# Kernel optimization log

Hardware: AMD Instinct MI355X
Metric: run time of the kernel (lower is better)

Reference implementation:

```python
import jax, jax.numpy as jnp
import numpy as np

N_NODES = 50000
N_EDGES = 800000
NODE_DIM = 128
EDGE_DIM = 16
OUT_DIM = 64
HEADS = 4


def setup_inputs() -> dict:
    key = jax.random.key(0)
    ks = jax.random.split(key, 12)
    x = jax.random.normal(ks[0], (N_NODES, NODE_DIM), jnp.float32)
    edge_index = jax.random.randint(ks[1], (2, N_EDGES), 0, N_NODES)
    batch = jnp.zeros((N_NODES,), jnp.int32)
    edge_attr = jax.random.normal(ks[2], (N_EDGES, EDGE_DIM), jnp.float32)
    s = 1.0 / np.sqrt(NODE_DIM)
    W = jax.random.normal(ks[3], (NODE_DIM, HEADS * OUT_DIM), jnp.float32) * s
    att_src = jax.random.normal(ks[4], (HEADS, OUT_DIM), jnp.float32) * 0.1
    att_dst = jax.random.normal(ks[5], (HEADS, OUT_DIM), jnp.float32) * 0.1
    W_e = jax.random.normal(ks[6], (EDGE_DIM, HEADS * OUT_DIM), jnp.float32) * (1.0 / np.sqrt(EDGE_DIM))
    att_edge = jax.random.normal(ks[7], (HEADS, OUT_DIM), jnp.float32) * 0.1
    bias = jnp.zeros((OUT_DIM,), jnp.float32)
    gamma = jnp.ones((OUT_DIM,), jnp.float32)
    beta = jnp.zeros((OUT_DIM,), jnp.float32)
    return {"x": x, "edge_index": edge_index, "batch": batch, "edge_attr": edge_attr,
            "W": W, "att_src": att_src, "att_dst": att_dst, "W_e": W_e,
            "att_edge": att_edge, "bias": bias, "gamma": gamma, "beta": beta}


def reference(x, edge_index, batch, edge_attr, W, att_src, att_dst, W_e, att_edge, bias, gamma, beta):
    N = x.shape[0]
    H, C = att_src.shape
    src, dst = edge_index[0], edge_index[1]
    E = src.shape[0]

    # add self loops; self-loop edge_attr = per-node mean of incoming edge attrs (PyG fill_value='mean')
    cnt = jax.ops.segment_sum(jnp.ones((E, 1), x.dtype), dst, num_segments=N)
    loop_attr = jax.ops.segment_sum(edge_attr, dst, num_segments=N) / jnp.maximum(cnt, 1.0)
    loop_idx = jnp.arange(N, dtype=src.dtype)
    src_f = jnp.concatenate([src, loop_idx])
    dst_f = jnp.concatenate([dst, loop_idx])
    ea = jnp.concatenate([edge_attr, loop_attr], axis=0)

    h = (x @ W).reshape(N, H, C)                       # [N,H,C]
    a_src = jnp.einsum('nhc,hc->nh', h, att_src)       # [N,H]
    a_dst = jnp.einsum('nhc,hc->nh', h, att_dst)
    e_emb = (ea @ W_e).reshape(-1, H, C)               # [E',H,C]
    a_edge = jnp.einsum('ehc,hc->eh', e_emb, att_edge)

    alpha = jax.nn.leaky_relu(a_src[src_f] + a_dst[dst_f] + a_edge, 0.2)  # [E',H]
    amax = jax.ops.segment_max(alpha, dst_f, num_segments=N)
    expa = jnp.exp(alpha - amax[dst_f])
    denom = jax.ops.segment_sum(expa, dst_f, num_segments=N)
    att = expa / (denom[dst_f] + 1e-16)                # segment softmax over dst

    msg = h[src_f] * att[:, :, None]                   # [E',H,C]
    out = jax.ops.segment_sum(msg, dst_f, num_segments=N)  # [N,H,C]
    out = out.mean(axis=1) + bias                      # concat=False -> head mean

    mu = out.mean(-1, keepdims=True)
    var = out.var(-1, keepdims=True)
    out = (out - mu) / jnp.sqrt(var + 1e-5) * gamma + beta
    return jax.nn.elu(out)
```

## Files before the change

kernel.cpp:

```cpp
#include <hip/hip_runtime.h>

typedef unsigned int u32;
typedef unsigned short u16;

static constexpr int NN  = 50000;
static constexpr int EE  = 800000;
static constexpr int CAP = 64;

typedef __attribute__((ext_vector_type(8))) short bf16x8;
typedef __attribute__((ext_vector_type(4))) float f32x4;

__device__ inline float u2f(u32 u){ union{u32 i; float f;} v; v.i=u; return v.f; }
__device__ inline float bf2f(u16 u){ return u2f(((u32)u)<<16); }
__device__ inline u16 f2bf(float f){ union{float f; u32 i;} v; v.f=f; u32 i=v.i;
    return (u16)((i + 0x7fffu + ((i>>16)&1u))>>16); }
__device__ inline u32 pk2(float a, float b){ return (u32)f2bf(a) | ((u32)f2bf(b)<<16); }
__device__ inline float lrelu(float x){ return x > 0.f ? x : 0.2f*x; }

__device__ inline float ld(const void* base, size_t i, int f32m){
    return f32m ? ((const float*)base)[i] : bf2f(((const u16*)base)[i]);
}

__device__ inline float wsum(float v){
    #pragma unroll
    for (int m=1;m<64;m<<=1) v += __shfl_xor(v, m, 64);
    return v;
}

#if defined(__has_builtin)
#if __has_builtin(__builtin_amdgcn_fdot2_f32_bf16)
#define HAS_DOT2 1
#endif
#endif

#ifdef HAS_DOT2
typedef __attribute__((ext_vector_type(2))) __bf16 bf16x2;
#endif

__device__ inline float dot2acc(u32 hv, u32 wv, float acc){
#ifdef HAS_DOT2
    union { u32 u; bf16x2 v; } a, b; a.u = hv; b.u = wv;
    return __builtin_amdgcn_fdot2_f32_bf16(a.v, b.v, acc, false);
#else
    acc = fmaf(u2f(hv<<16),         u2f(wv<<16),         acc);
    acc = fmaf(u2f(hv&0xffff0000u), u2f(wv&0xffff0000u), acc);
    return acc;
#endif
}

__device__ inline int detect_f32(const u16* xraw){
    int lane = threadIdx.x & 63;
    bool bad = false;
    #pragma unroll
    for (int i = 0; i < 8; ++i){
        float v = bf2f(xraw[2*(lane + i*64)]);
        if (!(fabsf(v) < 1e10f)) bad = true;
    }
    return __any(bad) ? 1 : 0;
}

__device__ inline void edge_logits(const void* ea, int e, int f32m,
                                   const float* Ml, float* A){
    float v[16];
    if (f32m){
        const float4* r = ((const float4*)ea) + (size_t)e*4;
        float4 a = r[0], b = r[1], c = r[2], d = r[3];
        v[0]=a.x; v[1]=a.y; v[2]=a.z; v[3]=a.w;
        v[4]=b.x; v[5]=b.y; v[6]=b.z; v[7]=b.w;
        v[8]=c.x; v[9]=c.y; v[10]=c.z; v[11]=c.w;
        v[12]=d.x; v[13]=d.y; v[14]=d.z; v[15]=d.w;
    } else {
        const uint4* r = ((const uint4*)ea) + (size_t)e*2;
        uint4 q0 = r[0], q1 = r[1];
        v[0]=u2f(q0.x<<16); v[1]=u2f(q0.x&0xffff0000u);
        v[2]=u2f(q0.y<<16); v[3]=u2f(q0.y&0xffff0000u);
        v[4]=u2f(q0.z<<16); v[5]=u2f(q0.z&0xffff0000u);
        v[6]=u2f(q0.w<<16); v[7]=u2f(q0.w&0xffff0000u);
        v[8]=u2f(q1.x<<16); v[9]=u2f(q1.x&0xffff0000u);
        v[10]=u2f(q1.y<<16); v[11]=u2f(q1.y&0xffff0000u);
        v[12]=u2f(q1.z<<16); v[13]=u2f(q1.z&0xffff0000u);
        v[14]=u2f(q1.w<<16); v[15]=u2f(q1.w&0xffff0000u);
    }
    float a0=0,a1=0,a2=0,a3=0;
    #pragma unroll
    for (int j = 0; j < 16; ++j){
        a0 = fmaf(v[j], Ml[j*4+0], a0);
        a1 = fmaf(v[j], Ml[j*4+1], a1);
        a2 = fmaf(v[j], Ml[j*4+2], a2);
        a3 = fmaf(v[j], Ml[j*4+3], a3);
    }
    A[0]=a0; A[1]=a1; A[2]=a2; A[3]=a3;
}

__global__ __launch_bounds__(256) void k_prep(const u16* __restrict__ xraw,
                                              const void* __restrict__ W,
                                              const void* __restrict__ att_src,
                                              const void* __restrict__ att_dst,
                                              const void* __restrict__ W_e,
                                              const void* __restrict__ att_edge,
                                              int* __restrict__ flag,
                                              u16* __restrict__ Wt,
                                              float* __restrict__ Mv){
    int f32m = detect_f32(xraw);
    int b = blockIdx.x, t = threadIdx.x;
    if (b == 0){
        if (t == 0) *flag = f32m;
        if (t < 64){
            int d = t >> 2, h = t & 3;
            float s = 0.f;
            for (int c = 0; c < 64; ++c)
                s += ld(W_e, d*256 + h*64 + c, f32m) * ld(att_edge, h*64 + c, f32m);
            Mv[t] = s;
        }
    } else if (b <= 128){
        int i = (b-1)*256 + t;
        int k = i >> 8, n = i & 255;
        Wt[n*128 + k] = f2bf(ld(W, (size_t)k*256 + n, f32m));
    } else {
        int i = (b-129)*256 + t;
        int c = i >> 7, k = i & 127;
        float s = 0.f;
        if (c < 8){
            int h = c & 3;
            const void* att = (c < 4) ? att_src : att_dst;
            for (int j = 0; j < 64; ++j)
                s += ld(W, (size_t)k*256 + h*64 + j, f32m) * ld(att, h*64 + j, f32m);
        }
        Wt[(size_t)(256 + c)*128 + k] = f2bf(s);
    }
}

static constexpr int LDSROW = 136;
static constexpr int CROW   = 264;

__global__ __launch_bounds__(256) void k_gemm(const void* __restrict__ x,
                                              const u16* __restrict__ Wt,
                                              const int* __restrict__ flag,
                                              u16* __restrict__ hbuf,
                                              float* __restrict__ a_src,
                                              float* __restrict__ a_dst, int N){
    __shared__ u16 sh[64*CROW];
    int f32m = *flag;
    int t = threadIdx.x;
    int row0 = blockIdx.x*64;
    if (f32m){
        const float4* xg = (const float4*)x;
        #pragma unroll
        for (int j=0;j<8;++j){
            int idx = t + j*256;
            int r = idx >> 5, c4 = idx & 31;
            int gr = row0 + r; if (gr >= N) gr = N-1;
            float4 v = xg[(size_t)gr*32 + c4];
            *(uint2*)&sh[r*LDSROW + c4*4] = make_uint2(pk2(v.x,v.y), pk2(v.z,v.w));
        }
    } else {
        const uint4* xg = (const uint4*)x;
        #pragma unroll
        for (int j=0;j<4;++j){
            int idx = t + j*256;
            int r = idx >> 4, c8 = idx & 15;
            int gr = row0 + r; if (gr >= N) gr = N-1;
            uint4 v = xg[(size_t)gr*16 + c8];
            *(uint4*)&sh[r*LDSROW + c8*8] = v;
        }
    }
    __syncthreads();
    int wave = t >> 6, lane = t & 63;
    int l15 = lane & 15, quad = lane >> 4;
    int mrow = wave*16 + l15;
    bf16x8 afr[4];
    #pragma unroll
    for (int s=0;s<4;++s)
        afr[s] = *(const bf16x8*)&sh[mrow*LDSROW + s*32 + quad*8];
    __syncthreads();
    f32x4 acc[17];
    #pragma unroll
    for (int tl=0;tl<17;++tl){
        f32x4 a = {0.f,0.f,0.f,0.f};
        #pragma unroll
        for (int s=0;s<4;++s){
            bf16x8 bfr = *(const bf16x8*)&Wt[(size_t)(tl*16 + l15)*128 + s*32 + quad*8];
            a = __builtin_amdgcn_mfma_f32_16x16x32_bf16(afr[s], bfr, a, 0, 0, 0);
        }
        acc[tl] = a;
    }
    int rbase = row0 + wave*16 + quad*4;
    #pragma unroll
    for (int r=0;r<4;++r){
        int gr = rbase + r;
        if (gr < N){
            if (l15 < 4)      a_src[gr*4 + l15]     = acc[16][r];
            else if (l15 < 8) a_dst[gr*4 + (l15-4)] = acc[16][r];
        }
    }
    #pragma unroll
    for (int r=0;r<4;++r){
        int row = wave*16 + quad*4 + r;
        #pragma unroll
        for (int tl=0;tl<4;++tl){
            u32 lo = pk2(acc[tl  ][r], acc[tl+4 ][r]);
            u32 hi = pk2(acc[tl+8][r], acc[tl+12][r]);
            *(uint2*)&sh[row*CROW + (tl*16 + l15)*4] = make_uint2(lo, hi);
        }
    }
    __syncthreads();
    uint4* h4 = (uint4*)hbuf;
    #pragma unroll
    for (int j=0;j<8;++j){
        int idx = t + j*256;
        int row = idx >> 5, c16 = idx & 31;
        if (row0 + row < N){
            uint4 v = *(const uint4*)&sh[row*CROW + c16*8];
            h4[(size_t)(row0 + row)*32 + c16] = v;
        }
    }
}

__global__ __launch_bounds__(256) void k_edge(const int* __restrict__ ei,
                                              const void* __restrict__ ea,
                                              const float* __restrict__ Mv,
                                              const int* __restrict__ flag,
                                              const float* __restrict__ a_src,
                                              const float* __restrict__ a_dst,
                                              int* __restrict__ deg,
                                              uint4* __restrict__ brec,
                                              u32* __restrict__ ba23, int E){
    __shared__ float Ml[64];
    if (threadIdx.x < 64) Ml[threadIdx.x] = Mv[threadIdx.x];
    __syncthreads();
    int f32m = *flag;
    int base = blockIdx.x*1024 + threadIdx.x;
    int e[4], src[4], dst[4];
    bool val[4];
    float A[4][4];
    #pragma unroll
    for (int j=0;j<4;++j){
        e[j] = base + j*256;
        val[j] = e[j] < E;
        int ec = val[j] ? e[j] : 0;
        src[j] = ei[ec];
        dst[j] = ei[E + ec];
        edge_logits(ea, ec, f32m, Ml, A[j]);
    }
    float4 as[4], ad[4];
    #pragma unroll
    for (int j=0;j<4;++j){
        as[j] = ((const float4*)a_src)[src[j]];
        ad[j] = ((const float4*)a_dst)[dst[j]];
    }
    #pragma unroll
    for (int j=0;j<4;++j){
        if (!val[j]) continue;
        float w0 = expf(lrelu(as[j].x + ad[j].x + A[j][0]));
        float w1 = expf(lrelu(as[j].y + ad[j].y + A[j][1]));
        float w2 = expf(lrelu(as[j].z + ad[j].z + A[j][2]));
        float w3 = expf(lrelu(as[j].w + ad[j].w + A[j][3]));
        int slot = atomicAdd(&deg[dst[j]], 1);
        if (slot < CAP){
            int idx = dst[j]*CAP + slot;
            brec[idx] = make_uint4((u32)src[j], pk2(w0,w1), pk2(w2,w3), pk2(A[j][0],A[j][1]));
            ba23[idx] = pk2(A[j][2],A[j][3]);
        }
    }
}

__global__ __launch_bounds__(256) void k_node(const int* __restrict__ deg,
                                              const uint4* __restrict__ brec,
                                              const u32* __restrict__ ba23,
                                              const float* __restrict__ a_src,
                                              const float* __restrict__ a_dst,
                                              const u16* __restrict__ hbuf,
                                              const void* __restrict__ bias,
                                              const void* __restrict__ gamma,
                                              const void* __restrict__ beta,
                                              const int* __restrict__ flag,
                                              void* __restrict__ out, int N){
    __shared__ uint4 lrec[4][CAP+4];
    int f32m = *flag;
    int lane = threadIdx.x & 63;
    int slot = threadIdx.x >> 6;
    int n = blockIdx.x*4 + slot;
    int dg = deg[n];
    int dc = dg < CAP ? dg : CAP;
    float4 an = ((const float4*)a_src)[n];
    float4 ad = ((const float4*)a_dst)[n];
    bool v0 = lane < dc;
    u32 src = (u32)n;
    float w0=0.f,w1=0.f,w2=0.f,w3=0.f;
    float a0=0.f,a1=0.f,a2=0.f,a3=0.f;
    if (v0){
        uint4 r = brec[(size_t)n*CAP + lane];
        u32 q = ba23[(size_t)n*CAP + lane];
        src = r.x;
        w0 = u2f(r.y<<16); w1 = u2f(r.y&0xffff0000u);
        w2 = u2f(r.z<<16); w3 = u2f(r.z&0xffff0000u);
        a0 = u2f(r.w<<16); a1 = u2f(r.w&0xffff0000u);
        a2 = u2f(q<<16);   a3 = u2f(q&0xffff0000u);
    }
    float dn0 = wsum(w0), dn1 = wsum(w1), dn2 = wsum(w2), dn3 = wsum(w3);
    float invd = 1.f / (float)(dg > 1 ? dg : 1);
    float ge0 = wsum(a0)*invd, ge1 = wsum(a1)*invd;
    float ge2 = wsum(a2)*invd, ge3 = wsum(a3)*invd;
    float exS0 = expf(lrelu(an.x + ad.x + ge0));
    float exS1 = expf(lrelu(an.y + ad.y + ge1));
    float exS2 = expf(lrelu(an.z + ad.z + ge2));
    float exS3 = expf(lrelu(an.w + ad.w + ge3));
    float i0 = 0.25f/(dn0 + exS0 + 1e-16f);
    float i1 = 0.25f/(dn1 + exS1 + 1e-16f);
    float i2 = 0.25f/(dn2 + exS2 + 1e-16f);
    float i3 = 0.25f/(dn3 + exS3 + 1e-16f);
    if (v0)
        lrec[slot][lane] = make_uint4(src, pk2(w0*i0, w1*i1), pk2(w2*i2, w3*i3), 0u);
    if (lane == 0)
        lrec[slot][dc] = make_uint4((u32)n, pk2(exS0*i0, exS1*i1), pk2(exS2*i2, exS3*i3), 0u);
    else if (lane <= 3)
        lrec[slot][dc + lane] = make_uint4((u32)n, 0u, 0u, 0u);
    __syncthreads();
    int T = dc + 1;
    int iters = (T + 3) >> 2;
    int half = lane >> 5, l5 = lane & 31;
    const uint4* hb4 = (const uint4*)hbuf;
    float acc0 = 0.f, acc1 = 0.f;
    uint4 r0 = lrec[slot][half];
    uint4 r1 = lrec[slot][2 + half];
    uint4 h0 = hb4[(size_t)r0.x*32 + l5];
    uint4 h1 = hb4[(size_t)r1.x*32 + l5];
    for (int i = 1; i < iters; ++i){
        uint4 nr0 = lrec[slot][4*i + half];
        uint4 nr1 = lrec[slot][4*i + 2 + half];
        uint4 nh0 = hb4[(size_t)nr0.x*32 + l5];
        uint4 nh1 = hb4[(size_t)nr1.x*32 + l5];
        acc0 = dot2acc(h0.x, r0.y, acc0);
        acc0 = dot2acc(h0.y, r0.z, acc0);
        acc1 = dot2acc(h0.z, r0.y, acc1);
        acc1 = dot2acc(h0.w, r0.z, acc1);
        acc0 = dot2acc(h1.x, r1.y, acc0);
        acc0 = dot2acc(h1.y, r1.z, acc0);
        acc1 = dot2acc(h1.z, r1.y, acc1);
        acc1 = dot2acc(h1.w, r1.z, acc1);
        r0 = nr0; r1 = nr1; h0 = nh0; h1 = nh1;
    }
    acc0 = dot2acc(h0.x, r0.y, acc0);
    acc0 = dot2acc(h0.y, r0.z, acc0);
    acc1 = dot2acc(h0.z, r0.y, acc1);
    acc1 = dot2acc(h0.w, r0.z, acc1);
    acc0 = dot2acc(h1.x, r1.y, acc0);
    acc0 = dot2acc(h1.y, r1.z, acc0);
    acc1 = dot2acc(h1.z, r1.y, acc1);
    acc1 = dot2acc(h1.w, r1.z, acc1);
    acc0 += __shfl_xor(acc0, 32, 64);
    acc1 += __shfl_xor(acc1, 32, 64);
    float va = __shfl(acc0, lane>>1, 64);
    float vb = __shfl(acc1, lane>>1, 64);
    float o = ((lane & 1) ? vb : va) + ld(bias, lane, f32m);
    float mu = wsum(o) * (1.f/64.f);
    float d = o - mu;
    float var = wsum(d*d) * (1.f/64.f);
    float y = d * rsqrtf(var + 1e-5f) * ld(gamma, lane, f32m) + ld(beta, lane, f32m);
    y = y > 0.f ? y : expf(y) - 1.f;
    if (f32m) ((float*)out)[(size_t)n*64 + lane] = y;
    else      ((u16*)out)[(size_t)n*64 + lane] = f2bf(y);
}

extern "C" void kernel_launch(void* const* d_in, const int* in_sizes, int n_in,
                              void* d_out, int out_size, void* d_ws, size_t ws_size,
                              hipStream_t stream){
    const void* x        = d_in[0];
    const int*  ei       = (const int*)d_in[1];
    const void* ea       = d_in[3];
    const void* W        = d_in[4];
    const void* att_src  = d_in[5];
    const void* att_dst  = d_in[6];
    const void* W_e      = d_in[7];
    const void* att_edge = d_in[8];
    const void* bias     = d_in[9];
    const void* gamma    = d_in[10];
    const void* beta     = d_in[11];
    const int N = NN, E = EE;

    char* p = (char*)d_ws;
    auto alloc = [&](size_t bytes){ void* r = (void*)p; p += (bytes + 255) & ~(size_t)255; return r; };
    int*   deg   = (int*)  alloc((size_t)N*4);
    float* Mv    = (float*)alloc(64*4);
    float* a_src = (float*)alloc((size_t)N*16);
    float* a_dst = (float*)alloc((size_t)N*16);
    uint4* brec  = (uint4*)alloc((size_t)N*CAP*16);
    u32*   ba23  = (u32*)  alloc((size_t)N*CAP*4);
    u16*   hbuf  = (u16*)  alloc((size_t)N*256*2);
    u16*   Wt    = (u16*)  alloc((size_t)272*128*2);
    int*   flag  = (int*)  alloc(256);

    hipMemsetAsync(deg, 0, (size_t)N*4, stream);
    k_prep<<<137, 256, 0, stream>>>((const u16*)x, W, att_src, att_dst, W_e, att_edge,
                                    flag, Wt, Mv);
    k_gemm<<<(N+63)/64, 256, 0, stream>>>(x, Wt, flag, hbuf, a_src, a_dst, N);
    k_edge<<<(E+1023)/1024, 256, 0, stream>>>(ei, ea, Mv, flag, a_src, a_dst,
                                              deg, brec, ba23, E);
    k_node<<<N/4, 256, 0, stream>>>(deg, brec, ba23, a_src, a_dst, hbuf,
                                    bias, gamma, beta, flag, d_out, N);
}
```

Measured before the change: 302.6 us.

## Move edge exp weights into node kernel and shrink bucket records to 12 bytes

The edge kernel no longer gathers a_src/a_dst or computes exp weights. It stores only src plus four fp16 edge logits per bucketed record, packed into 12 bytes instead of 16+4. The node kernel now gathers a_src[src] per edge and computes the exponentials there. Streaming inputs use nontemporal loads, and the edge kernel handles 2 edges per thread instead of 4. This cuts bucket write/read traffic and the random gathers in k_edge, at the cost of a random gather in k_node, unaligned 3-word records, and fp16 precision for the logits.

```diff
diff --git a/kernel.cpp b/kernel.cpp
--- a/kernel.cpp
+++ b/kernel.cpp
@@ -9,6 +9,7 @@
 
 typedef __attribute__((ext_vector_type(8))) short bf16x8;
 typedef __attribute__((ext_vector_type(4))) float f32x4;
+typedef __attribute__((ext_vector_type(4))) u32   u32x4;
 
 __device__ inline float u2f(u32 u){ union{u32 i; float f;} v; v.i=u; return v.f; }
 __device__ inline float bf2f(u16 u){ return u2f(((u32)u)<<16); }
@@ -16,6 +17,14 @@
     return (u16)((i + 0x7fffu + ((i>>16)&1u))>>16); }
 __device__ inline u32 pk2(float a, float b){ return (u32)f2bf(a) | ((u32)f2bf(b)<<16); }
 __device__ inline float lrelu(float x){ return x > 0.f ? x : 0.2f*x; }
+
+__device__ inline u32 pkh(float a, float b){
+    union{ _Float16 h[2]; u32 u; } v;
+    v.h[0] = (_Float16)a; v.h[1] = (_Float16)b;
+    return v.u;
+}
+__device__ inline float hlo(u32 u){ union{u32 u; _Float16 h[2];} v; v.u=u; return (float)v.h[0]; }
+__device__ inline float hhi(u32 u){ union{u32 u; _Float16 h[2];} v; v.u=u; return (float)v.h[1]; }
 
 __device__ inline float ld(const void* base, size_t i, int f32m){
     return f32m ? ((const float*)base)[i] : bf2f(((const u16*)base)[i]);
@@ -63,23 +72,27 @@
                                    const float* Ml, float* A){
     float v[16];
     if (f32m){
-        const float4* r = ((const float4*)ea) + (size_t)e*4;
-        float4 a = r[0], b = r[1], c = r[2], d = r[3];
-        v[0]=a.x; v[1]=a.y; v[2]=a.z; v[3]=a.w;
-        v[4]=b.x; v[5]=b.y; v[6]=b.z; v[7]=b.w;
-        v[8]=c.x; v[9]=c.y; v[10]=c.z; v[11]=c.w;
-        v[12]=d.x; v[13]=d.y; v[14]=d.z; v[15]=d.w;
+        const f32x4* r = ((const f32x4*)ea) + (size_t)e*4;
+        f32x4 a = __builtin_nontemporal_load(r);
+        f32x4 b = __builtin_nontemporal_load(r+1);
+        f32x4 c = __builtin_nontemporal_load(r+2);
+        f32x4 d = __builtin_nontemporal_load(r+3);
+        v[0]=a[0]; v[1]=a[1]; v[2]=a[2]; v[3]=a[3];
+        v[4]=b[0]; v[5]=b[1]; v[6]=b[2]; v[7]=b[3];
+        v[8]=c[0]; v[9]=c[1]; v[10]=c[2]; v[11]=c[3];
+        v[12]=d[0]; v[13]=d[1]; v[14]=d[2]; v[15]=d[3];
     } else {
-        const uint4* r = ((const uint4*)ea) + (size_t)e*2;
-        uint4 q0 = r[0], q1 = r[1];
-        v[0]=u2f(q0.x<<16); v[1]=u2f(q0.x&0xffff0000u);
-        v[2]=u2f(q0.y<<16); v[3]=u2f(q0.y&0xffff0000u);
-        v[4]=u2f(q0.z<<16); v[5]=u2f(q0.z&0xffff0000u);
-        v[6]=u2f(q0.w<<16); v[7]=u2f(q0.w&0xffff0000u);
-        v[8]=u2f(q1.x<<16); v[9]=u2f(q1.x&0xffff0000u);
-        v[10]=u2f(q1.y<<16); v[11]=u2f(q1.y&0xffff0000u);
-        v[12]=u2f(q1.z<<16); v[13]=u2f(q1.z&0xffff0000u);
-        v[14]=u2f(q1.w<<16); v[15]=u2f(q1.w&0xffff0000u);
+        const u32x4* r = ((const u32x4*)ea) + (size_t)e*2;
+        u32x4 q0 = __builtin_nontemporal_load(r);
+        u32x4 q1 = __builtin_nontemporal_load(r+1);
+        v[0]=u2f(q0[0]<<16); v[1]=u2f(q0[0]&0xffff0000u);
+        v[2]=u2f(q0[1]<<16); v[3]=u2f(q0[1]&0xffff0000u);
+        v[4]=u2f(q0[2]<<16); v[5]=u2f(q0[2]&0xffff0000u);
+        v[6]=u2f(q0[3]<<16); v[7]=u2f(q0[3]&0xffff0000u);
+        v[8]=u2f(q1[0]<<16); v[9]=u2f(q1[0]&0xffff0000u);
+        v[10]=u2f(q1[1]<<16); v[11]=u2f(q1[1]&0xffff0000u);
+        v[12]=u2f(q1[2]<<16); v[13]=u2f(q1[2]&0xffff0000u);
+        v[14]=u2f(q1[3]<<16); v[15]=u2f(q1[3]&0xffff0000u);
     }
     float a0=0,a1=0,a2=0,a3=0;
     #pragma unroll
@@ -144,24 +157,24 @@
     int t = threadIdx.x;
     int row0 = blockIdx.x*64;
     if (f32m){
-        const float4* xg = (const float4*)x;
+        const f32x4* xg = (const f32x4*)x;
         #pragma unroll
         for (int j=0;j<8;++j){
             int idx = t + j*256;
             int r = idx >> 5, c4 = idx & 31;
             int gr = row0 + r; if (gr >= N) gr = N-1;
-            float4 v = xg[(size_t)gr*32 + c4];
-            *(uint2*)&sh[r*LDSROW + c4*4] = make_uint2(pk2(v.x,v.y), pk2(v.z,v.w));
+            f32x4 v = __builtin_nontemporal_load(&xg[(size_t)gr*32 + c4]);
+            *(uint2*)&sh[r*LDSROW + c4*4] = make_uint2(pk2(v[0],v[1]), pk2(v[2],v[3]));
         }
     } else {
-        const uint4* xg = (const uint4*)x;
+        const u32x4* xg = (const u32x4*)x;
         #pragma unroll
         for (int j=0;j<4;++j){
             int idx = t + j*256;
             int r = idx >> 4, c8 = idx & 15;
             int gr = row0 + r; if (gr >= N) gr = N-1;
-            uint4 v = xg[(size_t)gr*16 + c8];
-            *(uint4*)&sh[r*LDSROW + c8*8] = v;
+            u32x4 v = __builtin_nontemporal_load(&xg[(size_t)gr*16 + c8]);
+            *(u32x4*)&sh[r*LDSROW + c8*8] = v;
         }
     }
     __syncthreads();
@@ -220,53 +233,33 @@
                                               const void* __restrict__ ea,
                                               const float* __restrict__ Mv,
                                               const int* __restrict__ flag,
-                                              const float* __restrict__ a_src,
-                                              const float* __restrict__ a_dst,
                                               int* __restrict__ deg,
-                                              uint4* __restrict__ brec,
-                                              u32* __restrict__ ba23, int E){
+                                              u32* __restrict__ brec, int E){
     __shared__ float Ml[64];
     if (threadIdx.x < 64) Ml[threadIdx.x] = Mv[threadIdx.x];
     __syncthreads();
     int f32m = *flag;
-    int base = blockIdx.x*1024 + threadIdx.x;
-    int e[4], src[4], dst[4];
-    bool val[4];
-    float A[4][4];
-    #pragma unroll
-    for (int j=0;j<4;++j){
-        e[j] = base + j*256;
-        val[j] = e[j] < E;
-        int ec = val[j] ? e[j] : 0;
-        src[j] = ei[ec];
-        dst[j] = ei[E + ec];
-        edge_logits(ea, ec, f32m, Ml, A[j]);
-    }
-    float4 as[4], ad[4];
-    #pragma unroll
-    for (int j=0;j<4;++j){
-        as[j] = ((const float4*)a_src)[src[j]];
-        ad[j] = ((const float4*)a_dst)[dst[j]];
-    }
-    #pragma unroll
-    for (int j=0;j<4;++j){
-        if (!val[j]) continue;
-        float w0 = expf(lrelu(as[j].x + ad[j].x + A[j][0]));
-        float w1 = expf(lrelu(as[j].y + ad[j].y + A[j][1]));
-        float w2 = expf(lrelu(as[j].z + ad[j].z + A[j][2]));
-        float w3 = expf(lrelu(as[j].w + ad[j].w + A[j][3]));
-        int slot = atomicAdd(&deg[dst[j]], 1);
+    int base = blockIdx.x*512 + threadIdx.x;
+    #pragma unroll
+    for (int j=0;j<2;++j){
+        int e = base + j*256;
+        if (e >= E) continue;
+        int src = __builtin_nontemporal_load(&ei[e]);
+        int dst = __builtin_nontemporal_load(&ei[E + e]);
+        float A[4];
+        edge_logits(ea, e, f32m, Ml, A);
+        int slot = atomicAdd(&deg[dst], 1);
         if (slot < CAP){
-            int idx = dst[j]*CAP + slot;
-            brec[idx] = make_uint4((u32)src[j], pk2(w0,w1), pk2(w2,w3), pk2(A[j][0],A[j][1]));
-            ba23[idx] = pk2(A[j][2],A[j][3]);
+            size_t i3 = ((size_t)dst*CAP + slot)*3;
+            brec[i3]   = (u32)src;
+            brec[i3+1] = pkh(A[0], A[1]);
+            brec[i3+2] = pkh(A[2], A[3]);
         }
     }
 }
 
 __global__ __launch_bounds__(256) void k_node(const int* __restrict__ deg,
-                                              const uint4* __restrict__ brec,
-                                              const u32* __restrict__ ba23,
+                                              const u32* __restrict__ brec,
                                               const float* __restrict__ a_src,
                                               const float* __restrict__ a_dst,
                                               const u16* __restrict__ hbuf,
@@ -282,29 +275,33 @@
     int n = blockIdx.x*4 + slot;
     int dg = deg[n];
     int dc = dg < CAP ? dg : CAP;
-    float4 an = ((const float4*)a_src)[n];
-    float4 ad = ((const float4*)a_dst)[n];
+    float4 an  = ((const float4*)a_src)[n];
+    float4 adn = ((const float4*)a_dst)[n];
     bool v0 = lane < dc;
     u32 src = (u32)n;
     float w0=0.f,w1=0.f,w2=0.f,w3=0.f;
     float a0=0.f,a1=0.f,a2=0.f,a3=0.f;
     if (v0){
-        uint4 r = brec[(size_t)n*CAP + lane];
-        u32 q = ba23[(size_t)n*CAP + lane];
-        src = r.x;
-        w0 = u2f(r.y<<16); w1 = u2f(r.y&0xffff0000u);
-        w2 = u2f(r.z<<16); w3 = u2f(r.z&0xffff0000u);
-        a0 = u2f(r.w<<16); a1 = u2f(r.w&0xffff0000u);
-        a2 = u2f(q<<16);   a3 = u2f(q&0xffff0000u);
+        const u32* rp = brec + ((size_t)n*CAP + lane)*3;
+        u32 s   = rp[0];
+        u32 p01 = rp[1];
+        u32 p23 = rp[2];
+        src = s;
+        a0 = hlo(p01); a1 = hhi(p01); a2 = hlo(p23); a3 = hhi(p23);
+        float4 asg = ((const float4*)a_src)[s];
+        w0 = expf(lrelu(asg.x + adn.x + a0));
+        w1 = expf(lrelu(asg.y + adn.y + a1));
+        w2 = expf(lrelu(asg.z + adn.z + a2));
+        w3 = expf(lrelu(asg.w + adn.w + a3));
     }
     float dn0 = wsum(w0), dn1 = wsum(w1), dn2 = wsum(w2), dn3 = wsum(w3);
     float invd = 1.f / (float)(dg > 1 ? dg : 1);
     float ge0 = wsum(a0)*invd, ge1 = wsum(a1)*invd;
     float ge2 = wsum(a2)*invd, ge3 = wsum(a3)*invd;
-    float exS0 = expf(lrelu(an.x + ad.x + ge0));
-    float exS1 = expf(lrelu(an.y + ad.y + ge1));
-    float exS2 = expf(lrelu(an.z + ad.z + ge2));
-    float exS3 = expf(lrelu(an.w + ad.w + ge3));
+    float exS0 = expf(lrelu(an.x + adn.x + ge0));
+    float exS1 = expf(lrelu(an.y + adn.y + ge1));
+    float exS2 = expf(lrelu(an.z + adn.z + ge2));
+    float exS3 = expf(lrelu(an.w + adn.w + ge3));
     float i0 = 0.25f/(dn0 + exS0 + 1e-16f);
     float i1 = 0.25f/(dn1 + exS1 + 1e-16f);
     float i2 = 0.25f/(dn2 + exS2 + 1e-16f);
@@ -384,8 +381,7 @@
     float* Mv    = (float*)alloc(64*4);
     float* a_src = (float*)alloc((size_t)N*16);
     float* a_dst = (float*)alloc((size_t)N*16);
-    uint4* brec  = (uint4*)alloc((size_t)N*CAP*16);
-    u32*   ba23  = (u32*)  alloc((size_t)N*CAP*4);
+    u32*   brec  = (u32*)  alloc((size_t)N*CAP*12);
     u16*   hbuf  = (u16*)  alloc((size_t)N*256*2);
     u16*   Wt    = (u16*)  alloc((size_t)272*128*2);
     int*   flag  = (int*)  alloc(256);
@@ -394,8 +390,7 @@
     k_prep<<<137, 256, 0, stream>>>((const u16*)x, W, att_src, att_dst, W_e, att_edge,
                                     flag, Wt, Mv);
     k_gemm<<<(N+63)/64, 256, 0, stream>>>(x, Wt, flag, hbuf, a_src, a_dst, N);
-    k_edge<<<(E+1023)/1024, 256, 0, stream>>>(ei, ea, Mv, flag, a_src, a_dst,
-                                              deg, brec, ba23, E);
-    k_node<<<N/4, 256, 0, stream>>>(deg, brec, ba23, a_src, a_dst, hbuf,
+    k_edge<<<(E+511)/512, 256, 0, stream>>>(ei, ea, Mv, flag, deg, brec, E);
+    k_node<<<N/4, 256, 0, stream>>>(deg, brec, a_src, a_dst, hbuf,
                                     bias, gamma, beta, flag, d_out, N);
 }
```

New measurement: 289.2 us. 1.05x faster.
